# Kernel optimization log

Hardware: AMD Instinct MI355X
Metric: run time of the kernel (lower is better)

Reference implementation:

```python
import jax, jax.numpy as jnp
import numpy as np

B, T, D, K = 4, 2048, 1024, 4

def setup_inputs() -> dict:
    key = jax.random.key(0)
    ks = jax.random.split(key, 4)
    u = jax.random.normal(ks[0], (B, T, D), dtype=jnp.float32)
    s0 = jnp.zeros((B, K, D), dtype=jnp.float32)
    W_in = jax.random.normal(ks[1], (K * D, D), dtype=jnp.float32) * (1.0 / np.sqrt(D))
    b_in = jnp.zeros((K * D,), dtype=jnp.float32)
    W_out = jax.random.normal(ks[2], (D, K * D), dtype=jnp.float32) * (1.0 / np.sqrt(K * D))
    b_out = jnp.zeros((D,), dtype=jnp.float32)
    decay_logit = jax.random.normal(ks[3], (K,), dtype=jnp.float32)
    return {"u": u, "s0": s0, "W_in": W_in, "b_in": b_in,
            "W_out": W_out, "b_out": b_out, "decay_logit": decay_logit}

def reference(u, s0, W_in, b_in, W_out, b_out, decay_logit):
    # u: (B,T,D); s0: (B,K,D)
    Bb, Tt, Dd = u.shape
    Kk = decay_logit.shape[0]
    # input projection -> (B,T,K,D) -> (T,B,K,D) for scan over time
    inp = (jnp.einsum('btd,ed->bte', u, W_in) + b_in).reshape(Bb, Tt, Kk, Dd)
    xs = jnp.transpose(inp, (1, 0, 2, 3))  # (T,B,K,D)
    decay = jax.nn.sigmoid(decay_logit).reshape(1, Kk, 1)  # (1,K,1)

    def step(s, x):
        s_next = decay * s + x
        return s_next, s_next

    s_last, s_seq = jax.lax.scan(step, s0, xs)  # s_seq: (T,B,K,D)
    g_in = jnp.transpose(s_seq, (1, 0, 2, 3)).reshape(Bb, Tt, Kk * Dd)
    g = jnp.einsum('bte,de->btd', g_in, W_out) + b_out
    return g, s_last
```

## Files before the change

### kernel.cpp

```cpp
#include <hip/hip_runtime.h>


#define Bb 4
#define Tt 2048
#define Dd 1024
#define Kk 4
#define BT (Bb*Tt)
#define Ee (Kk*Dd)
#define NCH 32
#define LCH 64

typedef __bf16 bf16x8 __attribute__((ext_vector_type(8)));
typedef float  f32x4  __attribute__((ext_vector_type(4)));

__device__ __forceinline__ float bf2f(ushort u){
  union { unsigned int i; float f; } x; x.i = ((unsigned int)u) << 16; return x.f;
}
__device__ __forceinline__ ushort f2bf(float f){
  union { unsigned int i; float f; } x; x.f = f;
  unsigned int i = x.i;
  return (ushort)((i + 0x7FFFu + ((i >> 16) & 1u)) >> 16);
}
__device__ __forceinline__ float sigm(float x){ return 1.0f / (1.0f + expf(-x)); }

__global__ __launch_bounds__(256) void k_f2bf4(const float4* __restrict__ in,
                                               ushort4* __restrict__ out, int n4){
  int i = blockIdx.x * 256 + threadIdx.x;
  if (i < n4){
    float4 v = in[i];
    ushort4 o; o.x = f2bf(v.x); o.y = f2bf(v.y); o.z = f2bf(v.z); o.w = f2bf(v.w);
    out[i] = o;
  }
}

__global__ __launch_bounds__(256) void k_transpose(const float* __restrict__ in,
                                                   ushort* __restrict__ out){
  __shared__ float tile[32][33];
  int tx = threadIdx.x, ty = threadIdx.y;
  int c0 = blockIdx.x * 32, r0 = blockIdx.y * 32;
  #pragma unroll
  for (int j = 0; j < 4; ++j)
    tile[ty + j*8][tx] = in[(size_t)(r0 + ty + j*8) * Dd + c0 + tx];
  __syncthreads();
  #pragma unroll
  for (int j = 0; j < 4; ++j)
    out[(size_t)(c0 + ty + j*8) * Ee + r0 + tx] = f2bf(tile[tx][ty + j*8]);
}

__global__ __launch_bounds__(256) void gemm_nt(const ushort* __restrict__ A,
                                               const ushort* __restrict__ B,
                                               ushort* __restrict__ C,
                                               int Kred, int lda, int ldb, int ldc,
                                               long aBatch, long bBatch, long cBatch){
  __shared__ ushort As[128 * 32];
  __shared__ ushort Bs[128 * 32];
  A += (long)blockIdx.z * aBatch;
  B += (long)blockIdx.z * bBatch;
  C += (long)blockIdx.z * cBatch;
  const int tid  = threadIdx.x;
  const int lane = tid & 63;
  const int w    = tid >> 6;
  const int wr   = w >> 1, wc = w & 1;
  const int rowBase = blockIdx.x * 128;
  const int colBase = blockIdx.y * 128;

  f32x4 acc[4][4] = {};
  const int krow = (lane >> 4) * 8;
  const int rsel = lane & 15;

  for (int kk = 0; kk < Kred; kk += 32){
    __syncthreads();
    #pragma unroll
    for (int i = 0; i < 2; ++i){
      int c  = i * 256 + tid;
      int r  = c >> 2;
      int c8 = (c & 3) * 8;
      const ushort* ga = A + (size_t)(rowBase + r) * lda + kk + c8;
      const ushort* gb = B + (size_t)(colBase + r) * ldb + kk + c8;
      __builtin_amdgcn_global_load_lds((const __attribute__((address_space(1))) void*)ga,
                                       (__attribute__((address_space(3))) void*)&As[c * 8],
                                       16, 0, 0);
      __builtin_amdgcn_global_load_lds((const __attribute__((address_space(1))) void*)gb,
                                       (__attribute__((address_space(3))) void*)&Bs[c * 8],
                                       16, 0, 0);
    }
    asm volatile("s_waitcnt vmcnt(0)" ::: "memory");
    __syncthreads();

    bf16x8 Af[4], Bf[4];
    #pragma unroll
    for (int mi = 0; mi < 4; ++mi)
      Af[mi] = *(const bf16x8*)&As[(wr*64 + mi*16 + rsel) * 32 + krow];
    #pragma unroll
    for (int ni = 0; ni < 4; ++ni)
      Bf[ni] = *(const bf16x8*)&Bs[(wc*64 + ni*16 + rsel) * 32 + krow];
    #pragma unroll
    for (int mi = 0; mi < 4; ++mi)
      #pragma unroll
      for (int ni = 0; ni < 4; ++ni)
        acc[mi][ni] = __builtin_amdgcn_mfma_f32_16x16x32_bf16(Af[mi], Bf[ni], acc[mi][ni], 0, 0, 0);
  }

  #pragma unroll
  for (int mi = 0; mi < 4; ++mi){
    #pragma unroll
    for (int ni = 0; ni < 4; ++ni){
      int r0 = rowBase + wr*64 + mi*16 + (lane >> 4) * 4;
      int c0 = colBase + wc*64 + ni*16 + (lane & 15);
      #pragma unroll
      for (int q = 0; q < 4; ++q)
        C[(size_t)(r0 + q) * ldc + c0] = f2bf(acc[mi][ni][q]);
    }
  }
}

#define STAGE_HALF(GB, LOFF)                                                   \
  { _Pragma("unroll")                                                          \
    for (int i_ = 0; i_ < 2; ++i_){                                            \
      int c_ = tid + i_*512;                                                   \
      int row_ = c_ >> 2;                                                      \
      int ss_ = (c_ & 3) ^ ((row_ >> 2) & 3);                                  \
      const ushort* g_ = (GB) + (size_t)row_ * 1024 + ss_ * 8;                 \
      __builtin_amdgcn_global_load_lds(                                        \
        (const __attribute__((address_space(1))) void*)g_,                     \
        (__attribute__((address_space(3))) void*)&lds[(LOFF) + c_*8],          \
        16, 0, 0);                                                             \
    } }

#define LOAD_A4(DST, KH, MH)                                                   \
  { _Pragma("unroll")                                                          \
    for (int mi_ = 0; mi_ < 4; ++mi_){                                         \
      int r_ = wm*128 + (MH)*64 + mi_*16 + rsel;                               \
      int uo_ = r_*32 + kq*8;                                                  \
      uo_ ^= ((uo_ >> 7) & 3) << 3;                                            \
      DST[mi_] = *(const bf16x8*)&lds[cbase + (KH)*8192 + uo_];                \
    } }

#define LOAD_B4(DST, KH)                                                       \
  { _Pragma("unroll")                                                          \
    for (int ni_ = 0; ni_ < 4; ++ni_){                                         \
      int r_ = wn*64 + ni_*16 + rsel;                                          \
      int uo_ = r_*32 + kq*8;                                                  \
      uo_ ^= ((uo_ >> 7) & 3) << 3;                                            \
      DST[ni_] = *(const bf16x8*)&lds[cbase + 16384 + (KH)*8192 + uo_];        \
    } }

#define MFMA16(MH, AARR, BARR)                                                 \
  { _Pragma("unroll")                                                          \
    for (int mi_ = 0; mi_ < 4; ++mi_)                                          \
      { _Pragma("unroll")                                                      \
        for (int ni_ = 0; ni_ < 4; ++ni_)                                      \
          acc[(MH)*4+mi_][ni_] = __builtin_amdgcn_mfma_f32_16x16x32_bf16(      \
              AARR[mi_], BARR[ni_], acc[(MH)*4+mi_][ni_], 0, 0, 0); } }

#define BAR() __builtin_amdgcn_s_barrier()

__global__ __launch_bounds__(512, 2) void gemm_big(const ushort* __restrict__ A,
                                                   const ushort* __restrict__ B,
                                                   ushort* __restrict__ C,
                                                   const float* __restrict__ dlog,
                                                   float* __restrict__ carry){
  __shared__ ushort lds[65536];
  const int tid  = threadIdx.x;
  const int lane = tid & 63;
  const int w    = tid >> 6;
  const int wm   = w >> 2;
  const int wn   = w & 3;
  const int rsel = lane & 15;
  const int kq   = lane >> 4;

  int bid = blockIdx.x;
  int xcd = bid & 7, rr = bid >> 3;
  const int rowBase = (((xcd >> 1) << 3) + (rr & 7)) * 256;
  const int colBase = (((xcd & 1) << 3) + (rr >> 3)) * 256;

  const ushort* Ag = A + (size_t)rowBase * 1024;
  const ushort* Bg = B + (size_t)colBase * 1024;

  f32x4 acc[8][4] = {};

  STAGE_HALF(Ag +  0, 0);
  STAGE_HALF(Bg +  0, 16384);
  STAGE_HALF(Ag + 32, 8192);
  STAGE_HALF(Bg + 32, 24576);
  STAGE_HALF(Ag + 64, 32768 + 0);
  STAGE_HALF(Bg + 64, 32768 + 16384);
  STAGE_HALF(Ag + 96, 32768 + 8192);
  STAGE_HALF(Bg + 96, 32768 + 24576);
  asm volatile("s_waitcnt vmcnt(8)" ::: "memory");
  BAR();

  for (int t = 0; t < 16; ++t){
    const int cbase = (t & 1) * 32768;
    bf16x8 am0[4], am1[4], bf0[4];
    LOAD_A4(am0, 0, 0); LOAD_B4(bf0, 0); LOAD_A4(am1, 0, 1);
    MFMA16(0, am0, bf0);
    MFMA16(1, am1, bf0);
    LOAD_A4(am0, 1, 0); LOAD_B4(bf0, 1); LOAD_A4(am1, 1, 1);
    MFMA16(0, am0, bf0);
    MFMA16(1, am1, bf0);
    asm volatile("s_waitcnt lgkmcnt(0)" ::: "memory");
    BAR();
    if (t < 14){
      STAGE_HALF(Ag + (t+2)*64,      cbase + 0);
      STAGE_HALF(Bg + (t+2)*64,      cbase + 16384);
      STAGE_HALF(Ag + (t+2)*64 + 32, cbase + 8192);
      STAGE_HALF(Bg + (t+2)*64 + 32, cbase + 24576);
      asm volatile("s_waitcnt vmcnt(8)" ::: "memory");
    } else {
      asm volatile("s_waitcnt vmcnt(0)" ::: "memory");
    }
    BAR();
  }

  #pragma unroll
  for (int mi = 0; mi < 8; ++mi){
    #pragma unroll
    for (int j = 0; j < 4; ++j){
      #pragma unroll
      for (int q = 0; q < 4; ++q){
        int row = wm*128 + mi*16 + (lane >> 4)*4 + q;
        int col = wn*64 + j*16 + rsel;
        int byte = row*512 + col*2;
        byte ^= ((row >> 2) & 3) << 5;
        *(ushort*)((char*)lds + byte) = f2bf(acc[mi][j][q]);
      }
    }
  }
  __syncthreads();

  {
    const int k_blk = colBase >> 10;
    const int b_blk = rowBase >> 11;
    const int ch0   = (rowBase & 2047) >> 6;
    const int d0    = colBase & 1023;
    const float p   = sigm(dlog[k_blk]);
    #pragma unroll
    for (int s = 0; s < 2; ++s){
      int task = tid + s*512;
      int col = task & 255, ch = task >> 8;
      float a = 0.f;
      for (int i = 0; i < 64; ++i){
        int row = ch*64 + i;
        int byte = row*512 + col*2;
        byte ^= ((row >> 2) & 3) << 5;
        a = p * a + bf2f(*(const ushort*)((char*)lds + byte));
      }
      carry[(size_t)((b_blk*Kk + k_blk)*NCH + ch0 + ch) * Dd + d0 + col] = a;
    }
  }

  #pragma unroll
  for (int j = 0; j < 16; ++j){
    int idx = tid + j*512;
    int r = idx >> 5, c8 = idx & 31;
    int byte = r*512 + c8*16;
    byte ^= ((r >> 2) & 3) << 5;
    f32x4 v = *(const f32x4*)((char*)lds + byte);
    *(f32x4*)&C[(size_t)(rowBase + r) * Ee + colBase + c8*8] = v;
  }
}

__global__ __launch_bounds__(256) void k_z0(const float* __restrict__ Wout,
                                            const float* __restrict__ s0,
                                            float* __restrict__ z0){
  int gid  = blockIdx.x * 4 + (threadIdx.x >> 6);
  int lane = threadIdx.x & 63;
  int d = gid & 1023, k = (gid >> 10) & 3, b = gid >> 12;
  const float* wrow = Wout + (size_t)d * Ee + k * Dd;
  const float* sv   = s0 + ((size_t)(b*Kk + k) << 10);
  float s = 0.f;
  #pragma unroll
  for (int j = 0; j < 16; ++j) s += wrow[lane + j*64] * sv[lane + j*64];
  for (int off = 32; off; off >>= 1) s += __shfl_down(s, off);
  if (lane == 0) z0[gid] = s;
}

__global__ __launch_bounds__(256) void k_cterm(const float* __restrict__ Wout,
                                               const float* __restrict__ b_in,
                                               float* __restrict__ cterm){
  int gid  = blockIdx.x * 4 + (threadIdx.x >> 6);
  int lane = threadIdx.x & 63;
  int d = gid & 1023, k = gid >> 10;
  const float* wrow = Wout + (size_t)d * Ee + k * Dd;
  const float* bv   = b_in + k * Dd;
  float s = 0.f;
  #pragma unroll
  for (int j = 0; j < 16; ++j) s += wrow[lane + j*64] * bv[lane + j*64];
  for (int off = 32; off; off >>= 1) s += __shfl_down(s, off);
  if (lane == 0) cterm[gid] = s;
}

__global__ __launch_bounds__(256) void k_scanInc(const float* __restrict__ carry,
                                                 const float* __restrict__ z0,
                                                 const float* __restrict__ dlog,
                                                 float* __restrict__ incoming){
  int idx = blockIdx.x * 256 + threadIdx.x;
  int k = (idx >> 10) & 3;
  int bk = idx >> 10, d = idx & 1023;
  float p  = sigm(dlog[k]);
  float dL = powf(p, (float)LCH);
  float inc = z0[idx];
  for (int c = 0; c < NCH; ++c){
    size_t o = ((size_t)(bk * NCH + c)) * Dd + d;
    incoming[o] = inc;
    inc = dL * inc + carry[o];
  }
}

__global__ __launch_bounds__(256) void k_scanB(const ushort* __restrict__ Y,
                                               const float* __restrict__ incoming,
                                               const float* __restrict__ dlog,
                                               const float* __restrict__ b_out,
                                               const float* __restrict__ cterm,
                                               float* __restrict__ g){
  int x = blockIdx.x;
  int d = blockIdx.y * 256 + threadIdx.x;
  int c = x & 31, b = x >> 5;
  float p[4], z[4], ct[4], pw[4];
  #pragma unroll
  for (int k = 0; k < 4; ++k){
    p[k]  = sigm(dlog[k]);
    z[k]  = incoming[((size_t)(((b*Kk + k))*NCH + c)) * Dd + d];
    float omp = fmaxf(1.0f - p[k], 1e-30f);
    ct[k] = cterm[k * Dd + d] / omp;
    pw[k] = powf(p[k], (float)(c * LCH + 1));
  }
  float bo = b_out[d];
  size_t ybase = ((size_t)(b*Tt + c*LCH)) * Ee + d;
  size_t gbase = ((size_t)(b*Tt + c*LCH)) * Dd + d;
  for (int i = 0; i < LCH; ++i){
    float acc = bo;
    #pragma unroll
    for (int k = 0; k < 4; ++k){
      z[k] = p[k] * z[k] + bf2f(Y[ybase + (size_t)k * Dd]);
      acc += z[k] + ct[k] * (1.0f - pw[k]);
      pw[k] *= p[k];
    }
    g[gbase] = acc;
    ybase += Ee; gbase += Dd;
  }
}

__global__ __launch_bounds__(256) void k_prep(const float* __restrict__ u,
                                              const float* __restrict__ dlog,
                                              float* __restrict__ vpart,
                                              ushort* __restrict__ U_bf){
  int x = blockIdx.x;
  int d = blockIdx.y * 256 + threadIdx.x;
  int c = x & 31, b = x >> 5;
  float p[4], a[4] = {0.f, 0.f, 0.f, 0.f};
  #pragma unroll
  for (int k = 0; k < 4; ++k) p[k] = sigm(dlog[k]);
  size_t ub = ((size_t)(b*Tt + c*LCH)) * Dd + d;
  for (int i = 0; i < LCH; ++i){
    float uv = u[ub];
    U_bf[ub] = f2bf(uv);
    #pragma unroll
    for (int k = 0; k < 4; ++k) a[k] = p[k] * a[k] + uv;
    ub += Dd;
  }
  #pragma unroll
  for (int k = 0; k < 4; ++k)
    vpart[(((size_t)x) * Kk + k) * Dd + d] = a[k];
}

__global__ __launch_bounds__(256) void k_vcomb(const float* __restrict__ vpart,
                                               const float* __restrict__ dlog,
                                               float* __restrict__ vfull){
  int idx = blockIdx.x * 256 + threadIdx.x;
  int k = (idx >> 10) & 3, b = idx >> 12, d = idx & 1023;
  float p  = sigm(dlog[k]);
  float dL = powf(p, (float)LCH);
  float v = 0.f;
  for (int c = 0; c < NCH; ++c)
    v = dL * v + vpart[(((size_t)(b*NCH + c)) * Kk + k) * Dd + d];
  vfull[idx] = v;
}

__global__ __launch_bounds__(256) void k_slast(const float* __restrict__ W_in,
                                               const float* __restrict__ vfull,
                                               const float* __restrict__ s0,
                                               const float* __restrict__ b_in,
                                               const float* __restrict__ dlog,
                                               float* __restrict__ out){
  int gid  = blockIdx.x * 4 + (threadIdx.x >> 6);
  int lane = threadIdx.x & 63;
  int d = gid & 1023, k = (gid >> 10) & 3, b = gid >> 12;
  const float* wrow = W_in + (size_t)(k*Dd + d) * Dd;
  const float* vv   = vfull + ((size_t)(b*Kk + k) << 10);
  float s = 0.f;
  #pragma unroll
  for (int j = 0; j < 16; ++j) s += wrow[lane + j*64] * vv[lane + j*64];
  for (int off = 32; off; off >>= 1) s += __shfl_down(s, off);
  if (lane == 0){
    float p  = sigm(dlog[k]);
    float pT = powf(p, (float)Tt);
    float omp = 1.0f - p;
    float geo = (omp < 1e-12f) ? (float)Tt : (1.0f - pT) / omp;
    out[gid] = pT * s0[gid] + s + b_in[k*Dd + d] * geo;
  }
}

extern "C" void kernel_launch(void* const* d_in, const int* in_sizes, int n_in,
                              void* d_out, int out_size, void* d_ws, size_t ws_size,
                              hipStream_t stream){
  const float* u     = (const float*)d_in[0];
  const float* s0    = (const float*)d_in[1];
  const float* W_in  = (const float*)d_in[2];
  const float* b_in  = (const float*)d_in[3];
  const float* W_out = (const float*)d_in[4];
  const float* b_out = (const float*)d_in[5];
  const float* dlog  = (const float*)d_in[6];

  float* g_out     = (float*)d_out;
  float* slast_out = g_out + (size_t)BT * Dd;

  char* ws = (char*)d_ws;
  if (ws_size < 115490816ull) return;
  ushort* U_bf    = (ushort*)(ws);
  ushort* WinT    = (ushort*)(ws + 16777216);
  ushort* Wout_bf = (ushort*)(ws + 25165824);
  ushort* Mcat    = (ushort*)(ws + 33554432);
  ushort* Y       = (ushort*)(ws + 41943040);
  float*  carry   = (float*)(ws + 109051904);
  float*  incoming= (float*)(ws + 111149056);
  float*  z0buf   = (float*)(ws + 113246208);
  float*  cterm   = (float*)(ws + 113311744);
  float*  vpart   = (float*)(ws + 113328128);
  float*  vfull   = (float*)(ws + 115425280);

  k_prep<<<dim3(128, 4), 256, 0, stream>>>(u, dlog, vpart, U_bf);
  k_f2bf4<<<4096, 256, 0, stream>>>((const float4*)W_out, (ushort4*)Wout_bf, Dd*Ee/4);
  k_transpose<<<dim3(32, 128), dim3(32, 8), 0, stream>>>(W_in, WinT);

  gemm_nt<<<dim3(8, 8, 4), 256, 0, stream>>>(Wout_bf, WinT, Mcat,
                                             1024, Ee, Ee, Dd,
                                             1024L, 1024L, 1048576L);
  gemm_big<<<512, 512, 0, stream>>>(U_bf, Mcat, Y, dlog, carry);

  k_z0<<<4096, 256, 0, stream>>>(W_out, s0, z0buf);
  k_cterm<<<1024, 256, 0, stream>>>(W_out, b_in, cterm);

  k_scanInc<<<64, 256, 0, stream>>>(carry, z0buf, dlog, incoming);
  k_scanB<<<dim3(128, 4), 256, 0, stream>>>(Y, incoming, dlog, b_out, cterm, g_out);

  k_vcomb<<<64, 256, 0, stream>>>(vpart, dlog, vfull);
  k_slast<<<4096, 256, 0, stream>>>(W_in, vfull, s0, b_in, dlog, slast_out);
}
```

Baseline: 169.4 us.

## Shrink big GEMM tile to 128x128 and read bf16 W_out in z0/cterm

```diff
diff --git a/kernel.cpp b/kernel.cpp
--- a/kernel.cpp
+++ b/kernel.cpp
@@ -20,6 +20,12 @@
   union { unsigned int i; float f; } x; x.f = f;
   unsigned int i = x.i;
   return (ushort)((i + 0x7FFFu + ((i >> 16) & 1u)) >> 16);
+}
+__device__ __forceinline__ float lo16(unsigned u){
+  union { unsigned i; float f; } x; x.i = u << 16; return x.f;
+}
+__device__ __forceinline__ float hi16(unsigned u){
+  union { unsigned i; float f; } x; x.i = u & 0xFFFF0000u; return x.f;
 }
 __device__ __forceinline__ float sigm(float x){ return 1.0f / (1.0f + expf(-x)); }
 
@@ -114,10 +120,10 @@
   }
 }
 
-#define STAGE_HALF(GB, LOFF)                                                   \
+#define STAGE_OP(GB, LOFF)                                                     \
   { _Pragma("unroll")                                                          \
     for (int i_ = 0; i_ < 2; ++i_){                                            \
-      int c_ = tid + i_*512;                                                   \
+      int c_ = tid + i_*256;                                                   \
       int row_ = c_ >> 2;                                                      \
       int ss_ = (c_ & 3) ^ ((row_ >> 2) & 3);                                  \
       const ushort* g_ = (GB) + (size_t)row_ * 1024 + ss_ * 8;                 \
@@ -127,86 +133,73 @@
         16, 0, 0);                                                             \
     } }
 
-#define LOAD_A4(DST, KH, MH)                                                   \
+#define LOAD_A4(DST)                                                           \
   { _Pragma("unroll")                                                          \
     for (int mi_ = 0; mi_ < 4; ++mi_){                                         \
-      int r_ = wm*128 + (MH)*64 + mi_*16 + rsel;                               \
+      int r_ = wm*64 + mi_*16 + rsel;                                          \
       int uo_ = r_*32 + kq*8;                                                  \
       uo_ ^= ((uo_ >> 7) & 3) << 3;                                            \
-      DST[mi_] = *(const bf16x8*)&lds[cbase + (KH)*8192 + uo_];                \
+      DST[mi_] = *(const bf16x8*)&lds[cbase + uo_];                            \
     } }
 
-#define LOAD_B4(DST, KH)                                                       \
+#define LOAD_B4(DST)                                                           \
   { _Pragma("unroll")                                                          \
     for (int ni_ = 0; ni_ < 4; ++ni_){                                         \
       int r_ = wn*64 + ni_*16 + rsel;                                          \
       int uo_ = r_*32 + kq*8;                                                  \
       uo_ ^= ((uo_ >> 7) & 3) << 3;                                            \
-      DST[ni_] = *(const bf16x8*)&lds[cbase + 16384 + (KH)*8192 + uo_];        \
+      DST[ni_] = *(const bf16x8*)&lds[cbase + 4096 + uo_];                     \
     } }
 
-#define MFMA16(MH, AARR, BARR)                                                 \
-  { _Pragma("unroll")                                                          \
-    for (int mi_ = 0; mi_ < 4; ++mi_)                                          \
-      { _Pragma("unroll")                                                      \
-        for (int ni_ = 0; ni_ < 4; ++ni_)                                      \
-          acc[(MH)*4+mi_][ni_] = __builtin_amdgcn_mfma_f32_16x16x32_bf16(      \
-              AARR[mi_], BARR[ni_], acc[(MH)*4+mi_][ni_], 0, 0, 0); } }
-
+#define XB(R) ((((R) & 3) ^ (((R) >> 2) & 3)) << 5)
 #define BAR() __builtin_amdgcn_s_barrier()
 
-__global__ __launch_bounds__(512, 2) void gemm_big(const ushort* __restrict__ A,
+__global__ __launch_bounds__(256, 4) void gemm_big(const ushort* __restrict__ A,
                                                    const ushort* __restrict__ B,
                                                    ushort* __restrict__ C,
                                                    const float* __restrict__ dlog,
                                                    float* __restrict__ carry){
-  __shared__ ushort lds[65536];
+  __shared__ ushort lds[16384];
   const int tid  = threadIdx.x;
   const int lane = tid & 63;
   const int w    = tid >> 6;
-  const int wm   = w >> 2;
-  const int wn   = w & 3;
+  const int wm   = w >> 1;
+  const int wn   = w & 1;
   const int rsel = lane & 15;
   const int kq   = lane >> 4;
 
   int bid = blockIdx.x;
   int xcd = bid & 7, rr = bid >> 3;
-  const int rowBase = (((xcd >> 1) << 3) + (rr & 7)) * 256;
-  const int colBase = (((xcd & 1) << 3) + (rr >> 3)) * 256;
+  const int rowBase = ((xcd >> 1) * 16 + (rr & 15)) * 128;
+  const int colBase = ((xcd & 1) * 16 + (rr >> 4)) * 128;
 
   const ushort* Ag = A + (size_t)rowBase * 1024;
   const ushort* Bg = B + (size_t)colBase * 1024;
 
-  f32x4 acc[8][4] = {};
-
-  STAGE_HALF(Ag +  0, 0);
-  STAGE_HALF(Bg +  0, 16384);
-  STAGE_HALF(Ag + 32, 8192);
-  STAGE_HALF(Bg + 32, 24576);
-  STAGE_HALF(Ag + 64, 32768 + 0);
-  STAGE_HALF(Bg + 64, 32768 + 16384);
-  STAGE_HALF(Ag + 96, 32768 + 8192);
-  STAGE_HALF(Bg + 96, 32768 + 24576);
-  asm volatile("s_waitcnt vmcnt(8)" ::: "memory");
+  f32x4 acc[4][4] = {};
+
+  STAGE_OP(Ag +  0, 0);
+  STAGE_OP(Bg +  0, 4096);
+  STAGE_OP(Ag + 32, 8192);
+  STAGE_OP(Bg + 32, 8192 + 4096);
+  asm volatile("s_waitcnt vmcnt(4)" ::: "memory");
   BAR();
 
-  for (int t = 0; t < 16; ++t){
-    const int cbase = (t & 1) * 32768;
-    bf16x8 am0[4], am1[4], bf0[4];
-    LOAD_A4(am0, 0, 0); LOAD_B4(bf0, 0); LOAD_A4(am1, 0, 1);
-    MFMA16(0, am0, bf0);
-    MFMA16(1, am1, bf0);
-    LOAD_A4(am0, 1, 0); LOAD_B4(bf0, 1); LOAD_A4(am1, 1, 1);
-    MFMA16(0, am0, bf0);
-    MFMA16(1, am1, bf0);
+  for (int t = 0; t < 32; ++t){
+    const int cbase = (t & 1) * 8192;
+    bf16x8 af[4], bf[4];
+    LOAD_A4(af); LOAD_B4(bf);
+    #pragma unroll
+    for (int mi = 0; mi < 4; ++mi)
+      #pragma unroll
+      for (int ni = 0; ni < 4; ++ni)
+        acc[mi][ni] = __builtin_amdgcn_mfma_f32_16x16x32_bf16(af[mi], bf[ni], acc[mi][ni], 0, 0, 0);
     asm volatile("s_waitcnt lgkmcnt(0)" ::: "memory");
     BAR();
-    if (t < 14){
-      STAGE_HALF(Ag + (t+2)*64,      cbase + 0);
-      STAGE_HALF(Bg + (t+2)*64,      cbase + 16384);
-      STAGE_HALF(Ag + (t+2)*64 + 32, cbase + 8192);
-      STAGE_HALF(Bg + (t+2)*64 + 32, cbase + 24576);
-      asm volatile("s_waitcnt vmcnt(8)" ::: "memory");
+    if (t < 30){
+      STAGE_OP(Ag + (t+2)*32, cbase);
+      STAGE_OP(Bg + (t+2)*32, cbase + 4096);
+      asm volatile("s_waitcnt vmcnt(4)" ::: "memory");
     } else {
       asm volatile("s_waitcnt vmcnt(0)" ::: "memory");
     }
@@ -214,79 +207,89 @@
   }
 
   #pragma unroll
-  for (int mi = 0; mi < 8; ++mi){
+  for (int mi = 0; mi < 4; ++mi){
     #pragma unroll
     for (int j = 0; j < 4; ++j){
       #pragma unroll
       for (int q = 0; q < 4; ++q){
-        int row = wm*128 + mi*16 + (lane >> 4)*4 + q;
+        int row = wm*64 + mi*16 + (lane >> 4)*4 + q;
         int col = wn*64 + j*16 + rsel;
-        int byte = row*512 + col*2;
-        byte ^= ((row >> 2) & 3) << 5;
+        int byte = (row*256 + col*2) ^ XB(row);
         *(ushort*)((char*)lds + byte) = f2bf(acc[mi][j][q]);
       }
     }
   }
   __syncthreads();
 
-  {
+  if (tid < 128){
     const int k_blk = colBase >> 10;
     const int b_blk = rowBase >> 11;
     const int ch0   = (rowBase & 2047) >> 6;
     const int d0    = colBase & 1023;
     const float p   = sigm(dlog[k_blk]);
-    #pragma unroll
-    for (int s = 0; s < 2; ++s){
-      int task = tid + s*512;
-      int col = task & 255, ch = task >> 8;
-      float a = 0.f;
-      for (int i = 0; i < 64; ++i){
-        int row = ch*64 + i;
-        int byte = row*512 + col*2;
-        byte ^= ((row >> 2) & 3) << 5;
-        a = p * a + bf2f(*(const ushort*)((char*)lds + byte));
-      }
-      carry[(size_t)((b_blk*Kk + k_blk)*NCH + ch0 + ch) * Dd + d0 + col] = a;
-    }
-  }
-
-  #pragma unroll
-  for (int j = 0; j < 16; ++j){
-    int idx = tid + j*512;
-    int r = idx >> 5, c8 = idx & 31;
-    int byte = r*512 + c8*16;
-    byte ^= ((r >> 2) & 3) << 5;
+    int cp = tid & 63, ch = tid >> 6;
+    float a0 = 0.f, a1 = 0.f;
+    for (int i = 0; i < 64; ++i){
+      int row = ch*64 + i;
+      int byte = (row*256 + cp*4) ^ XB(row);
+      unsigned v = *(const unsigned*)((char*)lds + byte);
+      a0 = p * a0 + lo16(v);
+      a1 = p * a1 + hi16(v);
+    }
+    float* cdst = &carry[(size_t)((b_blk*Kk + k_blk)*NCH + ch0 + ch) * Dd + d0 + cp*2];
+    cdst[0] = a0; cdst[1] = a1;
+  }
+
+  #pragma unroll
+  for (int j = 0; j < 8; ++j){
+    int idx = tid + j*256;
+    int r = idx >> 4, c16 = idx & 15;
+    int byte = (r*256 + c16*16) ^ XB(r);
     f32x4 v = *(const f32x4*)((char*)lds + byte);
-    *(f32x4*)&C[(size_t)(rowBase + r) * Ee + colBase + c8*8] = v;
-  }
-}
-
-__global__ __launch_bounds__(256) void k_z0(const float* __restrict__ Wout,
+    *(f32x4*)&C[(size_t)(rowBase + r) * Ee + colBase + c16*8] = v;
+  }
+}
+
+__global__ __launch_bounds__(256) void k_z0(const ushort* __restrict__ Wout_bf,
                                             const float* __restrict__ s0,
                                             float* __restrict__ z0){
   int gid  = blockIdx.x * 4 + (threadIdx.x >> 6);
   int lane = threadIdx.x & 63;
   int d = gid & 1023, k = (gid >> 10) & 3, b = gid >> 12;
-  const float* wrow = Wout + (size_t)d * Ee + k * Dd;
+  const ushort* wrow = Wout_bf + (size_t)d * Ee + k * Dd;
   const float* sv   = s0 + ((size_t)(b*Kk + k) << 10);
   float s = 0.f;
   #pragma unroll
-  for (int j = 0; j < 16; ++j) s += wrow[lane + j*64] * sv[lane + j*64];
+  for (int j = 0; j < 2; ++j){
+    int base = lane*8 + j*512;
+    uint4 wv = *(const uint4*)(wrow + base);
+    float4 sa = *(const float4*)(sv + base);
+    float4 sb = *(const float4*)(sv + base + 4);
+    s += lo16(wv.x)*sa.x + hi16(wv.x)*sa.y + lo16(wv.y)*sa.z + hi16(wv.y)*sa.w
+       + lo16(wv.z)*sb.x + hi16(wv.z)*sb.y + lo16(wv.w)*sb.z + hi16(wv.w)*sb.w;
+  }
   for (int off = 32; off; off >>= 1) s += __shfl_down(s, off);
   if (lane == 0) z0[gid] = s;
 }
 
-__global__ __launch_bounds__(256) void k_cterm(const float* __restrict__ Wout,
+__global__ __launch_bounds__(256) void k_cterm(const ushort* __restrict__ Wout_bf,
                                                const float* __restrict__ b_in,
                                                float* __restrict__ cterm){
   int gid  = blockIdx.x * 4 + (threadIdx.x >> 6);
   int lane = threadIdx.x & 63;
   int d = gid & 1023, k = gid >> 10;
-  const float* wrow = Wout + (size_t)d * Ee + k * Dd;
+  const ushort* wrow = Wout_bf + (size_t)d * Ee + k * Dd;
   const float* bv   = b_in + k * Dd;
   float s = 0.f;
   #pragma unroll
-  for (int j = 0; j < 16; ++j) s += wrow[lane + j*64] * bv[lane + j*64];
+  for (int j = 0; j < 2; ++j){
+    int base = lane*8 + j*512;
+    uint4 wv = *(const uint4*)(wrow + base);
+    float4 sa = *(const float4*)(bv + base);
+    float4 sb = *(const float4*)(bv + base + 4);
+    s += lo16(wv.x)*sa.x + hi16(wv.x)*sa.y + lo16(wv.y)*sa.z + hi16(wv.y)*sa.w
+       + lo16(wv.z)*sb.x + hi16(wv.z)*sb.y + lo16(wv.w)*sb.z + hi16(wv.w)*sb.w;
+  }
   for (int off = 32; off; off >>= 1) s += __shfl_down(s, off);
   if (lane == 0) cterm[gid] = s;
 }
@@ -437,10 +440,10 @@
   gemm_nt<<<dim3(8, 8, 4), 256, 0, stream>>>(Wout_bf, WinT, Mcat,
                                              1024, Ee, Ee, Dd,
                                              1024L, 1024L, 1048576L);
-  gemm_big<<<512, 512, 0, stream>>>(U_bf, Mcat, Y, dlog, carry);
-
-  k_z0<<<4096, 256, 0, stream>>>(W_out, s0, z0buf);
-  k_cterm<<<1024, 256, 0, stream>>>(W_out, b_in, cterm);
+  gemm_big<<<2048, 256, 0, stream>>>(U_bf, Mcat, Y, dlog, carry);
+
+  k_z0<<<4096, 256, 0, stream>>>(Wout_bf, s0, z0buf);
+  k_cterm<<<1024, 256, 0, stream>>>(Wout_bf, b_in, cterm);
 
   k_scanInc<<<64, 256, 0, stream>>>(carry, z0buf, dlog, incoming);
   k_scanB<<<dim3(128, 4), 256, 0, stream>>>(Y, incoming, dlog, b_out, cterm, g_out);
```

New measurement: 173.7 us. +2.5%, slower.
